# Optimization experiments

Measured on AMD Instinct MI355X. Metric: run time of the kernel, lower is better.

## Reference

```python
import jax, jax.numpy as jnp
import numpy as np

DEPTH = 8
IN_FEATURES = 512
OUT_FEATURES = 256
LEAF_COUNT = 2 ** DEPTH          # 256
GATE_COUNT = LEAF_COUNT - 1      # 255
BATCH = 65536


def setup_inputs() -> dict:
    key = jax.random.key(0)
    k1, k2, k3 = jax.random.split(key, 3)
    x = jax.random.normal(k1, (BATCH, IN_FEATURES), dtype=jnp.float32)
    # gw stored transposed as (in_features, gate_count), kaiming-like scale
    gw = jax.random.normal(k2, (IN_FEATURES, GATE_COUNT), dtype=jnp.float32) * (1.0 / np.sqrt(IN_FEATURES))
    gb = jnp.zeros((GATE_COUNT,), dtype=jnp.float32)
    z = jax.random.normal(k3, (OUT_FEATURES, LEAF_COUNT), dtype=jnp.float32)
    return {"x": x, "gw": gw, "gb": gb, "z": z}


def _leaf_probs(x, gw, gb):
    # gatings: (B, gate_count); node it's left child (2p+1) uses g, right child (2p+2) uses 1-g
    g = jax.nn.sigmoid(x @ gw + gb)
    B = x.shape[0]
    dens = jnp.ones((B, 1), dtype=x.dtype)
    for d in range(DEPTH):  # level-wise vectorized traversal, O(depth) steps
        lo, hi = 2 ** d - 1, 2 ** (d + 1) - 1
        gl = g[:, lo:hi]  # (B, 2^d) gatings at this level
        # interleave [parent*g, parent*(1-g)] -> children order matches heap layout
        dens = jnp.stack([dens * gl, dens * (1.0 - gl)], axis=-1).reshape(B, -1)
    return dens  # (B, leaf_count)


def reference(x, gw, gb, z):
    leaf = _leaf_probs(x, gw, gb)        # (B, L)
    # constant projection: z @ leaf_probs^T, then transpose -> (B, out)
    return leaf @ z.T
```

## Files before the change

### kernel.cpp

```cpp
#include <hip/hip_runtime.h>
#include <hip/hip_bf16.h>
#include <stdint.h>


typedef short bf16x8 __attribute__((ext_vector_type(8)));
typedef float f32x4  __attribute__((ext_vector_type(4)));

__device__ __forceinline__ unsigned short f2bf(float f) {
    union { float f; uint32_t u; } c; c.f = f;
    uint32_t u = c.u;
    return (unsigned short)((u + 0x7FFFu + ((u >> 16) & 1u)) >> 16);
}

__device__ __forceinline__ uint32_t pkbf(float a, float b) {
    union { __hip_bfloat162 h; uint32_t u; } cv;
    cv.h = __float22bfloat162_rn(make_float2(a, b));
    return cv.u;
}

__global__ __launch_bounds__(256) void softtree_prep(
    const float* __restrict__ gw, const float* __restrict__ z,
    unsigned short* __restrict__ gwt, unsigned short* __restrict__ zb)
{
    if (blockIdx.x < 32) {
        __shared__ float tsm[64][65];
        const int k0 = (blockIdx.x >> 2) * 64;
        const int n0 = (blockIdx.x & 3) * 64;
        const int r = threadIdx.x >> 6;
        const int c = threadIdx.x & 63;
        const int n = n0 + c;
        #pragma unroll
        for (int i = 0; i < 16; ++i) {
            int kk = r + i * 4;
            tsm[kk][c] = (n < 255) ? gw[(size_t)(k0 + kk) * 255 + n] : 0.0f;
        }
        __syncthreads();
        #pragma unroll
        for (int i = 0; i < 16; ++i) {
            int nn = r + i * 4;
            gwt[(size_t)(n0 + nn) * 512 + k0 + c] = f2bf(tsm[c][nn]);
        }
    } else {
        int base = (blockIdx.x - 32) * 1024 + threadIdx.x * 4;
        const float4 v = *(const float4*)(z + base);
        ushort4 o;
        o.x = f2bf(v.x); o.y = f2bf(v.y); o.z = f2bf(v.z); o.w = f2bf(v.w);
        *(ushort4*)(zb + base) = o;
    }
}

__global__ __launch_bounds__(512, 4) void softtree_main(
    const float* __restrict__ x, const float* __restrict__ gb,
    const unsigned short* __restrict__ gwt, const unsigned short* __restrict__ zb,
    float* __restrict__ out)
{
    __shared__ char smraw[81920];
    float* gs = (float*)smraw;

    const int tid  = threadIdx.x;
    const int lane = tid & 63;
    const int wv   = tid >> 6;
    const int q    = lane >> 4;
    const int l15  = lane & 15;
    const int wr   = wv & 3;
    const int wc   = wv >> 2;
    const int R0   = blockIdx.x * 128;

    const int xrow = tid >> 3;
    const int xkg  = (tid & 7) ^ (xrow & 7);
    const float* xp0 = x + (size_t)(R0 + xrow) * 512 + xkg * 8;
    const float* xp1 = xp0 + (size_t)64 * 512;
    char* xsw0 = smraw + 65536 + tid * 16;
    char* xsw1 = xsw0 + 8192;

    const int ggate_b = wv * 32 + (lane >> 3);
    const int gkg     = (lane & 7) ^ ((lane >> 3) & 7);
    const unsigned short* gwp[4];
    #pragma unroll
    for (int j = 0; j < 4; ++j)
        gwp[j] = gwt + (size_t)(ggate_b + j * 8) * 512 + gkg * 8;
    const uint32_t gwLds = (uint32_t)(wv * 4) * 1024;

    f32x4 acc[2][8];
    #pragma unroll
    for (int t = 0; t < 2; ++t)
        #pragma unroll
        for (int i = 0; i < 8; ++i) acc[t][i] = (f32x4){0.f, 0.f, 0.f, 0.f};

    float4 xa0 = *(const float4*)(xp0);
    float4 xb0 = *(const float4*)(xp0 + 4);
    float4 xa1 = *(const float4*)(xp1);
    float4 xb1 = *(const float4*)(xp1 + 4);
    #pragma unroll
    for (int j = 0; j < 4; ++j)
        __builtin_amdgcn_global_load_lds(
            (const __attribute__((address_space(1))) void*)(gwp[j]),
            (__attribute__((address_space(3))) void*)(smraw + gwLds + j * 1024),
            16, 0, 0);

    for (int kc = 0; kc < 8; ++kc) {
        const int buf = kc & 1;
        __syncthreads();

        union { uint4 u4; uint32_t u[4]; } w0, w1;
        w0.u[0] = pkbf(xa0.x, xa0.y); w0.u[1] = pkbf(xa0.z, xa0.w);
        w0.u[2] = pkbf(xb0.x, xb0.y); w0.u[3] = pkbf(xb0.z, xb0.w);
        w1.u[0] = pkbf(xa1.x, xa1.y); w1.u[1] = pkbf(xa1.z, xa1.w);
        w1.u[2] = pkbf(xb1.x, xb1.y); w1.u[3] = pkbf(xb1.z, xb1.w);
        *(uint4*)xsw0 = w0.u4;
        *(uint4*)xsw1 = w1.u4;

        __syncthreads();

        if (kc < 7) {
            const int ko = (kc + 1) * 64;
            #pragma unroll
            for (int j = 0; j < 4; ++j)
                __builtin_amdgcn_global_load_lds(
                    (const __attribute__((address_space(1))) void*)(gwp[j] + ko),
                    (__attribute__((address_space(3))) void*)(smraw + (buf ^ 1) * 32768 + gwLds + j * 1024),
                    16, 0, 0);
            xa0 = *(const float4*)(xp0 + ko);
            xb0 = *(const float4*)(xp0 + ko + 4);
            xa1 = *(const float4*)(xp1 + ko);
            xb1 = *(const float4*)(xp1 + ko + 4);
        }

        #pragma unroll
        for (int s = 0; s < 2; ++s) {
            const int jx = (4 * s + q) ^ (l15 & 7);
            bf16x8 a0 = *(const bf16x8*)(smraw + 65536 + ((16 * wr + l15) * 8 + jx) * 16);
            bf16x8 a1 = *(const bf16x8*)(smraw + 65536 + 8192 + ((16 * wr + l15) * 8 + jx) * 16);
            #pragma unroll
            for (int nt = 0; nt < 8; ++nt) {
                const int gate = 128 * wc + nt * 16 + l15;
                bf16x8 b = *(const bf16x8*)(smraw + buf * 32768 + (gate * 8 + jx) * 16);
                acc[0][nt] = __builtin_amdgcn_mfma_f32_16x16x32_bf16(a0, b, acc[0][nt], 0, 0, 0);
                acc[1][nt] = __builtin_amdgcn_mfma_f32_16x16x32_bf16(a1, b, acc[1][nt], 0, 0, 0);
            }
        }
    }

    float gbv[8];
    #pragma unroll
    for (int nt = 0; nt < 8; ++nt) {
        int col = 128 * wc + nt * 16 + l15;
        gbv[nt] = (col < 255) ? gb[col] : 0.0f;
    }

    for (int t = 0; t < 2; ++t) {
        __syncthreads();

        #pragma unroll
        for (int nt = 0; nt < 8; ++nt) {
            const int col = 128 * wc + nt * 16 + l15;
            #pragma unroll
            for (int r = 0; r < 4; ++r) {
                const int rowl = 16 * wr + 4 * q + r;
                float v = acc[t][nt][r] + gbv[nt];
                gs[rowl * 258 + col] = 1.0f / (1.0f + __expf(-v));
            }
        }
        __syncthreads();

        const float* gr = gs + (16 * wr + l15) * 258;
        float g0v = gr[0];
        float t1v[2] = { g0v, 1.0f - g0v };
        float t2v[4], t3v[8];
        #pragma unroll
        for (int u = 0; u < 2; ++u) {
            float gl = gr[1 + u];
            t2v[2 * u] = t1v[u] * gl; t2v[2 * u + 1] = t1v[u] - t2v[2 * u];
        }
        #pragma unroll
        for (int u = 0; u < 4; ++u) {
            float gl = gr[3 + u];
            t3v[2 * u] = t2v[u] * gl; t3v[2 * u + 1] = t2v[u] - t3v[2 * u];
        }
        bf16x8 a2[8];
        #pragma unroll
        for (int c = 0; c < 8; ++c) {
            const int G = c * 4 + q;
            float p = t3v[c];
            float g3 = gr[7 + c];
            p = (q & 2) ? (p - p * g3) : (p * g3);
            float g4 = gr[15 + 2 * c + (q >> 1)];
            p = (q & 1) ? (p - p * g4) : (p * g4);
            float g5 = gr[31 + G];
            float a0 = p * g5, a1 = p - a0;
            float g6a = gr[63 + 2 * G], g6b = gr[64 + 2 * G];
            float b00 = a0 * g6a, b01 = a0 - b00;
            float b10 = a1 * g6b, b11 = a1 - b10;
            float g70 = gr[127 + 4 * G], g71 = gr[128 + 4 * G];
            float g72 = gr[129 + 4 * G], g73 = gr[130 + 4 * G];
            float lf0 = b00 * g70, lf1 = b00 - lf0;
            float lf2 = b01 * g71, lf3 = b01 - lf2;
            float lf4 = b10 * g72, lf5 = b10 - lf4;
            float lf6 = b11 * g73, lf7 = b11 - lf6;
            union { bf16x8 v; uint32_t u[4]; } pk;
            pk.u[0] = pkbf(lf0, lf1);
            pk.u[1] = pkbf(lf2, lf3);
            pk.u[2] = pkbf(lf4, lf5);
            pk.u[3] = pkbf(lf6, lf7);
            a2[c] = pk.v;
        }

        f32x4 acc2[8];
        #pragma unroll
        for (int i = 0; i < 8; ++i) acc2[i] = (f32x4){0.f, 0.f, 0.f, 0.f};
        #pragma unroll
        for (int nt = 0; nt < 8; ++nt) {
            const unsigned short* zrow = zb + (size_t)(128 * wc + nt * 16 + l15) * 256 + q * 8;
            #pragma unroll
            for (int c = 0; c < 8; ++c) {
                bf16x8 b = *(const bf16x8*)(zrow + c * 32);
                acc2[nt] = __builtin_amdgcn_mfma_f32_16x16x32_bf16(a2[c], b, acc2[nt], 0, 0, 0);
            }
        }

        #pragma unroll
        for (int nt = 0; nt < 8; ++nt) {
            const int col = 128 * wc + nt * 16 + l15;
            #pragma unroll
            for (int r = 0; r < 4; ++r) {
                const int row = R0 + t * 64 + 16 * wr + 4 * q + r;
                out[(size_t)row * 256 + col] = acc2[nt][r];
            }
        }
    }
}

extern "C" void kernel_launch(void* const* d_in, const int* in_sizes, int n_in,
                              void* d_out, int out_size, void* d_ws, size_t ws_size,
                              hipStream_t stream) {
    const float* x  = (const float*)d_in[0];
    const float* gw = (const float*)d_in[1];
    const float* gb = (const float*)d_in[2];
    const float* z  = (const float*)d_in[3];
    float* outp = (float*)d_out;

    unsigned short* gwt = (unsigned short*)d_ws;
    unsigned short* zbf = gwt + 256 * 512;

    softtree_prep<<<96, 256, 0, stream>>>(gw, z, gwt, zbf);
    softtree_main<<<512, 512, 0, stream>>>(x, gb, gwt, zbf, outp);
}
```

Measured before the change: 281.6 us.

## Halve row tile, load x directly to registers, store gates as bf16

Each block now handles 64 rows instead of 128, and the grid doubles to 1024 blocks. x is loaded straight from global memory into MFMA A-fragments rather than staged through shared memory. The gw tile goes through registers into a single LDS buffer, replacing the double-buffered async global_load_lds. Gate values are kept in LDS as bf16, which shrinks shared memory from 80KB to about 34KB so more blocks can be resident. The cost is that gw is reloaded twice as often per row, the LDS tile now has to be filled and synchronised every k-step, and the gates lose precision.

```diff
diff --git a/kernel.cpp b/kernel.cpp
--- a/kernel.cpp
+++ b/kernel.cpp
@@ -11,7 +11,9 @@
     uint32_t u = c.u;
     return (unsigned short)((u + 0x7FFFu + ((u >> 16) & 1u)) >> 16);
 }
-
+__device__ __forceinline__ float bf2f(unsigned short h) {
+    union { uint32_t u; float f; } c; c.u = ((uint32_t)h) << 16; return c.f;
+}
 __device__ __forceinline__ uint32_t pkbf(float a, float b) {
     union { __hip_bfloat162 h; uint32_t u; } cv;
     cv.h = __float22bfloat162_rn(make_float2(a, b));
@@ -54,8 +56,8 @@
     const unsigned short* __restrict__ gwt, const unsigned short* __restrict__ zb,
     float* __restrict__ out)
 {
-    __shared__ char smraw[81920];
-    float* gs = (float*)smraw;
+    __shared__ char smraw[64 * 266 * 2];
+    unsigned short* gs = (unsigned short*)smraw;
 
     const int tid  = threadIdx.x;
     const int lane = tid & 63;
@@ -64,168 +66,147 @@
     const int l15  = lane & 15;
     const int wr   = wv & 3;
     const int wc   = wv >> 2;
-    const int R0   = blockIdx.x * 128;
-
-    const int xrow = tid >> 3;
-    const int xkg  = (tid & 7) ^ (xrow & 7);
-    const float* xp0 = x + (size_t)(R0 + xrow) * 512 + xkg * 8;
-    const float* xp1 = xp0 + (size_t)64 * 512;
-    char* xsw0 = smraw + 65536 + tid * 16;
-    char* xsw1 = xsw0 + 8192;
-
-    const int ggate_b = wv * 32 + (lane >> 3);
-    const int gkg     = (lane & 7) ^ ((lane >> 3) & 7);
-    const unsigned short* gwp[4];
-    #pragma unroll
-    for (int j = 0; j < 4; ++j)
-        gwp[j] = gwt + (size_t)(ggate_b + j * 8) * 512 + gkg * 8;
-    const uint32_t gwLds = (uint32_t)(wv * 4) * 1024;
-
-    f32x4 acc[2][8];
-    #pragma unroll
-    for (int t = 0; t < 2; ++t)
-        #pragma unroll
-        for (int i = 0; i < 8; ++i) acc[t][i] = (f32x4){0.f, 0.f, 0.f, 0.f};
-
-    float4 xa0 = *(const float4*)(xp0);
-    float4 xb0 = *(const float4*)(xp0 + 4);
-    float4 xa1 = *(const float4*)(xp1);
-    float4 xb1 = *(const float4*)(xp1 + 4);
-    #pragma unroll
-    for (int j = 0; j < 4; ++j)
-        __builtin_amdgcn_global_load_lds(
-            (const __attribute__((address_space(1))) void*)(gwp[j]),
-            (__attribute__((address_space(3))) void*)(smraw + gwLds + j * 1024),
-            16, 0, 0);
+    const int R0   = blockIdx.x * 64;
+    const int row  = R0 + 16 * wr + l15;
+
+    const int g0 = tid >> 3;
+    const int kg = tid & 7;
+    const unsigned short* gsrc0 = gwt + (size_t)g0 * 512 + kg * 8;
+    char* gdst0 = smraw + (g0 * 8 + (kg ^ (g0 & 7))) * 16;
+
+    const float* xp = x + (size_t)row * 512 + q * 8;
+
+    const char* bb0 = smraw + (128 * wc + l15) * 128 + (((4 * 0 + q) ^ (l15 & 7)) * 16);
+    const char* bb1 = smraw + (128 * wc + l15) * 128 + (((4 * 1 + q) ^ (l15 & 7)) * 16);
+
+    f32x4 acc[8];
+    #pragma unroll
+    for (int i = 0; i < 8; ++i) acc[i] = (f32x4){0.f, 0.f, 0.f, 0.f};
+
+    uint4 gr4[4];
+    #pragma unroll
+    for (int j = 0; j < 4; ++j) gr4[j] = *(const uint4*)(gsrc0 + j * 32768);
+    float4 xc0 = *(const float4*)(xp);
+    float4 xc1 = *(const float4*)(xp + 4);
+    float4 xc2 = *(const float4*)(xp + 32);
+    float4 xc3 = *(const float4*)(xp + 36);
 
     for (int kc = 0; kc < 8; ++kc) {
-        const int buf = kc & 1;
+        #pragma unroll
+        for (int j = 0; j < 4; ++j) *(uint4*)(gdst0 + j * 8192) = gr4[j];
         __syncthreads();
 
-        union { uint4 u4; uint32_t u[4]; } w0, w1;
-        w0.u[0] = pkbf(xa0.x, xa0.y); w0.u[1] = pkbf(xa0.z, xa0.w);
-        w0.u[2] = pkbf(xb0.x, xb0.y); w0.u[3] = pkbf(xb0.z, xb0.w);
-        w1.u[0] = pkbf(xa1.x, xa1.y); w1.u[1] = pkbf(xa1.z, xa1.w);
-        w1.u[2] = pkbf(xb1.x, xb1.y); w1.u[3] = pkbf(xb1.z, xb1.w);
-        *(uint4*)xsw0 = w0.u4;
-        *(uint4*)xsw1 = w1.u4;
-
-        __syncthreads();
+        bf16x8 afr[2];
+        {
+            union { bf16x8 v; uint32_t u[4]; } pk;
+            pk.u[0] = pkbf(xc0.x, xc0.y); pk.u[1] = pkbf(xc0.z, xc0.w);
+            pk.u[2] = pkbf(xc1.x, xc1.y); pk.u[3] = pkbf(xc1.z, xc1.w);
+            afr[0] = pk.v;
+            pk.u[0] = pkbf(xc2.x, xc2.y); pk.u[1] = pkbf(xc2.z, xc2.w);
+            pk.u[2] = pkbf(xc3.x, xc3.y); pk.u[3] = pkbf(xc3.z, xc3.w);
+            afr[1] = pk.v;
+        }
 
         if (kc < 7) {
             const int ko = (kc + 1) * 64;
             #pragma unroll
-            for (int j = 0; j < 4; ++j)
-                __builtin_amdgcn_global_load_lds(
-                    (const __attribute__((address_space(1))) void*)(gwp[j] + ko),
-                    (__attribute__((address_space(3))) void*)(smraw + (buf ^ 1) * 32768 + gwLds + j * 1024),
-                    16, 0, 0);
-            xa0 = *(const float4*)(xp0 + ko);
-            xb0 = *(const float4*)(xp0 + ko + 4);
-            xa1 = *(const float4*)(xp1 + ko);
-            xb1 = *(const float4*)(xp1 + ko + 4);
-        }
-
-        #pragma unroll
-        for (int s = 0; s < 2; ++s) {
-            const int jx = (4 * s + q) ^ (l15 & 7);
-            bf16x8 a0 = *(const bf16x8*)(smraw + 65536 + ((16 * wr + l15) * 8 + jx) * 16);
-            bf16x8 a1 = *(const bf16x8*)(smraw + 65536 + 8192 + ((16 * wr + l15) * 8 + jx) * 16);
-            #pragma unroll
-            for (int nt = 0; nt < 8; ++nt) {
-                const int gate = 128 * wc + nt * 16 + l15;
-                bf16x8 b = *(const bf16x8*)(smraw + buf * 32768 + (gate * 8 + jx) * 16);
-                acc[0][nt] = __builtin_amdgcn_mfma_f32_16x16x32_bf16(a0, b, acc[0][nt], 0, 0, 0);
-                acc[1][nt] = __builtin_amdgcn_mfma_f32_16x16x32_bf16(a1, b, acc[1][nt], 0, 0, 0);
-            }
-        }
-    }
-
-    float gbv[8];
+            for (int j = 0; j < 4; ++j) gr4[j] = *(const uint4*)(gsrc0 + j * 32768 + ko);
+            xc0 = *(const float4*)(xp + ko);
+            xc1 = *(const float4*)(xp + ko + 4);
+            xc2 = *(const float4*)(xp + ko + 32);
+            xc3 = *(const float4*)(xp + ko + 36);
+        }
+
+        #pragma unroll
+        for (int nt = 0; nt < 8; ++nt) {
+            bf16x8 b0 = *(const bf16x8*)(bb0 + nt * 2048);
+            acc[nt] = __builtin_amdgcn_mfma_f32_16x16x32_bf16(afr[0], b0, acc[nt], 0, 0, 0);
+        }
+        #pragma unroll
+        for (int nt = 0; nt < 8; ++nt) {
+            bf16x8 b1 = *(const bf16x8*)(bb1 + nt * 2048);
+            acc[nt] = __builtin_amdgcn_mfma_f32_16x16x32_bf16(afr[1], b1, acc[nt], 0, 0, 0);
+        }
+        __syncthreads();
+    }
+
     #pragma unroll
     for (int nt = 0; nt < 8; ++nt) {
-        int col = 128 * wc + nt * 16 + l15;
-        gbv[nt] = (col < 255) ? gb[col] : 0.0f;
-    }
-
-    for (int t = 0; t < 2; ++t) {
-        __syncthreads();
-
-        #pragma unroll
-        for (int nt = 0; nt < 8; ++nt) {
-            const int col = 128 * wc + nt * 16 + l15;
-            #pragma unroll
-            for (int r = 0; r < 4; ++r) {
-                const int rowl = 16 * wr + 4 * q + r;
-                float v = acc[t][nt][r] + gbv[nt];
-                gs[rowl * 258 + col] = 1.0f / (1.0f + __expf(-v));
-            }
-        }
-        __syncthreads();
-
-        const float* gr = gs + (16 * wr + l15) * 258;
-        float g0v = gr[0];
-        float t1v[2] = { g0v, 1.0f - g0v };
-        float t2v[4], t3v[8];
+        const int col = 128 * wc + nt * 16 + l15;
+        const float gbv = (col < 255) ? gb[col] : 0.0f;
+        #pragma unroll
+        for (int r = 0; r < 4; ++r) {
+            const int rowl = 16 * wr + 4 * q + r;
+            float v = acc[nt][r] + gbv;
+            gs[rowl * 266 + col] = f2bf(1.0f / (1.0f + __expf(-v)));
+        }
+    }
+    __syncthreads();
+
+    const unsigned short* gr = gs + (16 * wr + l15) * 266;
+    float t1v[2], t2v[4], t3v[8];
+    {
+        float g0v = bf2f(gr[0]);
+        t1v[0] = g0v; t1v[1] = 1.0f - g0v;
         #pragma unroll
         for (int u = 0; u < 2; ++u) {
-            float gl = gr[1 + u];
+            float gl = bf2f(gr[1 + u]);
             t2v[2 * u] = t1v[u] * gl; t2v[2 * u + 1] = t1v[u] - t2v[2 * u];
         }
         #pragma unroll
         for (int u = 0; u < 4; ++u) {
-            float gl = gr[3 + u];
+            float gl = bf2f(gr[3 + u]);
             t3v[2 * u] = t2v[u] * gl; t3v[2 * u + 1] = t2v[u] - t3v[2 * u];
         }
-        bf16x8 a2[8];
+    }
+    bf16x8 a2[8];
+    #pragma unroll
+    for (int c = 0; c < 8; ++c) {
+        const int G = c * 4 + q;
+        float p = t3v[c];
+        float g3 = bf2f(gr[7 + c]);
+        p = (q & 2) ? (p - p * g3) : (p * g3);
+        float g4 = bf2f(gr[15 + 2 * c + (q >> 1)]);
+        p = (q & 1) ? (p - p * g4) : (p * g4);
+        float g5 = bf2f(gr[31 + G]);
+        float a0 = p * g5, a1 = p - a0;
+        float g6a = bf2f(gr[63 + 2 * G]), g6b = bf2f(gr[64 + 2 * G]);
+        float b00 = a0 * g6a, b01 = a0 - b00;
+        float b10 = a1 * g6b, b11 = a1 - b10;
+        float g70 = bf2f(gr[127 + 4 * G]), g71 = bf2f(gr[128 + 4 * G]);
+        float g72 = bf2f(gr[129 + 4 * G]), g73 = bf2f(gr[130 + 4 * G]);
+        float lf0 = b00 * g70, lf1 = b00 - lf0;
+        float lf2 = b01 * g71, lf3 = b01 - lf2;
+        float lf4 = b10 * g72, lf5 = b10 - lf4;
+        float lf6 = b11 * g73, lf7 = b11 - lf6;
+        union { bf16x8 v; uint32_t u[4]; } pk;
+        pk.u[0] = pkbf(lf0, lf1);
+        pk.u[1] = pkbf(lf2, lf3);
+        pk.u[2] = pkbf(lf4, lf5);
+        pk.u[3] = pkbf(lf6, lf7);
+        a2[c] = pk.v;
+    }
+
+    f32x4 acc2[8];
+    #pragma unroll
+    for (int i = 0; i < 8; ++i) acc2[i] = (f32x4){0.f, 0.f, 0.f, 0.f};
+    #pragma unroll
+    for (int nt = 0; nt < 8; ++nt) {
+        const unsigned short* zrow = zb + (size_t)(128 * wc + nt * 16 + l15) * 256 + q * 8;
         #pragma unroll
         for (int c = 0; c < 8; ++c) {
-            const int G = c * 4 + q;
-            float p = t3v[c];
-            float g3 = gr[7 + c];
-            p = (q & 2) ? (p - p * g3) : (p * g3);
-            float g4 = gr[15 + 2 * c + (q >> 1)];
-            p = (q & 1) ? (p - p * g4) : (p * g4);
-            float g5 = gr[31 + G];
-            float a0 = p * g5, a1 = p - a0;
-            float g6a = gr[63 + 2 * G], g6b = gr[64 + 2 * G];
-            float b00 = a0 * g6a, b01 = a0 - b00;
-            float b10 = a1 * g6b, b11 = a1 - b10;
-            float g70 = gr[127 + 4 * G], g71 = gr[128 + 4 * G];
-            float g72 = gr[129 + 4 * G], g73 = gr[130 + 4 * G];
-            float lf0 = b00 * g70, lf1 = b00 - lf0;
-            float lf2 = b01 * g71, lf3 = b01 - lf2;
-            float lf4 = b10 * g72, lf5 = b10 - lf4;
-            float lf6 = b11 * g73, lf7 = b11 - lf6;
-            union { bf16x8 v; uint32_t u[4]; } pk;
-            pk.u[0] = pkbf(lf0, lf1);
-            pk.u[1] = pkbf(lf2, lf3);
-            pk.u[2] = pkbf(lf4, lf5);
-            pk.u[3] = pkbf(lf6, lf7);
-            a2[c] = pk.v;
-        }
-
-        f32x4 acc2[8];
-        #pragma unroll
-        for (int i = 0; i < 8; ++i) acc2[i] = (f32x4){0.f, 0.f, 0.f, 0.f};
-        #pragma unroll
-        for (int nt = 0; nt < 8; ++nt) {
-            const unsigned short* zrow = zb + (size_t)(128 * wc + nt * 16 + l15) * 256 + q * 8;
-            #pragma unroll
-            for (int c = 0; c < 8; ++c) {
-                bf16x8 b = *(const bf16x8*)(zrow + c * 32);
-                acc2[nt] = __builtin_amdgcn_mfma_f32_16x16x32_bf16(a2[c], b, acc2[nt], 0, 0, 0);
-            }
-        }
-
-        #pragma unroll
-        for (int nt = 0; nt < 8; ++nt) {
-            const int col = 128 * wc + nt * 16 + l15;
-            #pragma unroll
-            for (int r = 0; r < 4; ++r) {
-                const int row = R0 + t * 64 + 16 * wr + 4 * q + r;
-                out[(size_t)row * 256 + col] = acc2[nt][r];
-            }
+            bf16x8 b = *(const bf16x8*)(zrow + c * 32);
+            acc2[nt] = __builtin_amdgcn_mfma_f32_16x16x32_bf16(a2[c], b, acc2[nt], 0, 0, 0);
+        }
+    }
+
+    #pragma unroll
+    for (int nt = 0; nt < 8; ++nt) {
+        const int col = 128 * wc + nt * 16 + l15;
+        #pragma unroll
+        for (int r = 0; r < 4; ++r) {
+            const int orow = R0 + 16 * wr + 4 * q + r;
+            out[(size_t)orow * 256 + col] = acc2[nt][r];
         }
     }
 }
@@ -243,5 +224,5 @@
     unsigned short* zbf = gwt + 256 * 512;
 
     softtree_prep<<<96, 256, 0, stream>>>(gw, z, gwt, zbf);
-    softtree_main<<<512, 512, 0, stream>>>(x, gb, gwt, zbf, outp);
-}
+    softtree_main<<<1024, 512, 0, stream>>>(x, gb, gwt, zbf, outp);
+}
```

Result: slower. 339.3 us (+20.5%).
